# Performance work log

Measured on AMD Instinct MI355X. Metric: run time of the kernel, lower is better.

## Reference

```python
import jax, jax.numpy as jnp
import numpy as np

B, T, D, H, Dh, DF, MH = 4, 1024, 1024, 16, 64, 4096, 256
EPS = 1e-6


def setup_inputs() -> dict:
    key = jax.random.key(0)
    ks = jax.random.split(key, 10)
    s = 0.02
    w = lambda k, shape: jax.random.normal(k, shape, jnp.float32) * s
    return {
        "x": jax.random.normal(ks[0], (B, T, D), jnp.float32),
        "norm1_w": jnp.ones((D,), jnp.float32),
        "norm2_w": jnp.ones((D,), jnp.float32),
        "wq": w(ks[1], (D, D)),
        "wk": w(ks[2], (D, D)),
        "wv": w(ks[3], (D, D)),
        "wo": w(ks[4], (D, D)),
        "mnet_w1": w(ks[5], (D, MH)),
        "mnet_w2": w(ks[6], (MH, H * Dh)),
        "gate_w": w(ks[7], (D, DF)),
        "up_w": w(ks[8], (D, DF)),
        "down_w": w(ks[9], (DF, D)),
    }


def _rmsnorm(x, w):
    rms = jnp.sqrt(jnp.mean(x * x, axis=-1, keepdims=True) + EPS)
    return w * (x / rms)


def reference(x, norm1_w, norm2_w, wq, wk, wv, wo, mnet_w1, mnet_w2, gate_w, up_w, down_w):
    # --- pre-norm geodesic (DRM) attention ---
    h = _rmsnorm(x, norm1_w)  # [B,T,D]
    q = (h @ wq).reshape(B, T, H, Dh)
    k = (h @ wk).reshape(B, T, H, Dh)
    v = (h @ wv).reshape(B, T, H, Dh)
    # MetricNet: positive diagonal metric G(x) per token/head
    g = jax.nn.softplus(jax.nn.silu(h @ mnet_w1) @ mnet_w2).reshape(B, T, H, Dh)
    # squared geodesic distance under key-side diagonal metric, expanded form:
    # dist_ij = sum_d g_jd*(q_id - k_jd)^2 = q^2.g - 2 q.(g*k) + sum(g*k^2)
    gk = g * k
    dist = (
        jnp.einsum("bihd,bjhd->bhij", q * q, g)
        - 2.0 * jnp.einsum("bihd,bjhd->bhij", q, gk)
        + jnp.transpose(jnp.sum(gk * k, axis=-1), (0, 2, 1))[:, :, None, :]
    )  # [B,H,T,T]
    scores = -dist / np.float32(np.sqrt(Dh))
    causal = jnp.tril(jnp.ones((T, T), bool))
    scores = jnp.where(causal, scores, jnp.float32(-1e30))
    attn = jax.nn.softmax(scores, axis=-1)
    o = jnp.einsum("bhij,bjhd->bihd", attn, v).reshape(B, T, D) @ wo
    x = x + o
    # --- pre-norm SwiGLU FFN ---
    h2 = _rmsnorm(x, norm2_w)
    ffn = (jax.nn.silu(h2 @ gate_w) * (h2 @ up_w)) @ down_w
    return x + ffn
```

## Files before the change

kernel.cpp:

```cpp
#include <hip/hip_runtime.h>
#include <hip/hip_bf16.h>
#include <math.h>

#define BB  4
#define TT  1024
#define DD  1024
#define HH  16
#define DH  64
#define DFF 4096
#define MHH 256

typedef __attribute__((ext_vector_type(8))) short bf16x8;
typedef __attribute__((ext_vector_type(4))) float f32x4;
typedef unsigned int u32;

#define NEG_BIG (-1e9f)

__device__ __forceinline__ float b2f(short s) {
    union { unsigned int u; float f; } x;
    x.u = ((unsigned int)(unsigned short)s) << 16;
    return x.f;
}
__device__ __forceinline__ short f2b(float f) {
    union { float f; unsigned int u; } x; x.f = f;
    unsigned int r = x.u + 0x7fffu + ((x.u >> 16) & 1u);
    return (short)(r >> 16);
}
__device__ __forceinline__ float silu_f(float x) { return x / (1.f + __expf(-x)); }

__device__ __forceinline__ void gld16(const short* g, short* l) {
    __builtin_amdgcn_global_load_lds(
        (const __attribute__((address_space(1))) u32*)g,
        (__attribute__((address_space(3))) u32*)l, 16, 0, 0);
}

#define STAGE64(ga0, ga1, lds, kb)                                  \
    {                                                               \
        gld16((ga0) + (kb),      &(lds)[tid * 8]);                  \
        gld16((ga1) + (kb),      &(lds)[2048 + tid * 8]);           \
        gld16((ga0) + (kb) + 32, &(lds)[4096 + tid * 8]);           \
        gld16((ga1) + (kb) + 32, &(lds)[4096 + 2048 + tid * 8]);    \
    }

__device__ __forceinline__ void convT_tile_body(
    const float* __restrict__ src, short* __restrict__ dst,
    int K, int N, int bx, int by, int tid, short (*Ts)[36])
{
    const int k0 = by * 32, n0 = bx * 32;
    const int r = tid >> 3, c4 = (tid & 7) * 4;
    float4 v = *(const float4*)(src + (size_t)(k0 + r) * N + n0 + c4);
    Ts[r][c4 + 0] = f2b(v.x); Ts[r][c4 + 1] = f2b(v.y);
    Ts[r][c4 + 2] = f2b(v.z); Ts[r][c4 + 3] = f2b(v.w);
    __syncthreads();
    short4 o;
    o.x = Ts[c4 + 0][r]; o.y = Ts[c4 + 1][r];
    o.z = Ts[c4 + 2][r]; o.w = Ts[c4 + 3][r];
    *(short4*)(dst + (size_t)(n0 + r) * K + k0 + c4) = o;
}

__global__ __launch_bounds__(256) void convT_pre_k(
    const float* __restrict__ wq, const float* __restrict__ wk,
    const float* __restrict__ wv, const float* __restrict__ mw1,
    const float* __restrict__ wo, const float* __restrict__ mw2,
    short* __restrict__ WfT, short* __restrict__ woT, short* __restrict__ mw2T)
{
    __shared__ __align__(16) short Ts[32][36];
    const int b = blockIdx.x, tid = threadIdx.x;
    const float* src; short* dst; int K, N, bx, by;
    if (b < 1024)      { src = wq;  dst = WfT;               K = DD;  N = DD;  int l = b;        bx = l & 31; by = l >> 5; }
    else if (b < 2048) { src = wk;  dst = WfT + 1024 * 1024; K = DD;  N = DD;  int l = b - 1024; bx = l & 31; by = l >> 5; }
    else if (b < 3072) { src = wv;  dst = WfT + 2048 * 1024; K = DD;  N = DD;  int l = b - 2048; bx = l & 31; by = l >> 5; }
    else if (b < 3328) { src = mw1; dst = WfT + 3072 * 1024; K = DD;  N = MHH; int l = b - 3072; bx = l & 7;  by = l >> 3; }
    else if (b < 4352) { src = wo;  dst = woT;               K = DD;  N = DD;  int l = b - 3328; bx = l & 31; by = l >> 5; }
    else               { src = mw2; dst = mw2T;              K = MHH; N = DD;  int l = b - 4352; bx = l & 31; by = l >> 5; }
    convT_tile_body(src, dst, K, N, bx, by, tid, Ts);
}

__global__ __launch_bounds__(256) void convT_ffn_k(
    const float* __restrict__ gw, const float* __restrict__ uw,
    const float* __restrict__ dw,
    short* __restrict__ WgT, short* __restrict__ WuT, short* __restrict__ WdT)
{
    __shared__ __align__(16) short Ts[32][36];
    const int b = blockIdx.x, tid = threadIdx.x;
    const float* src; short* dst; int K, N, bx, by;
    if (b < 4096)      { src = gw; dst = WgT; K = DD;  N = DFF; int l = b;        bx = l & 127; by = l >> 7; }
    else if (b < 8192) { src = uw; dst = WuT; K = DD;  N = DFF; int l = b - 4096; bx = l & 127; by = l >> 7; }
    else               { src = dw; dst = WdT; K = DFF; N = DD;  int l = b - 8192; bx = l & 31;  by = l >> 5; }
    convT_tile_body(src, dst, K, N, bx, by, tid, Ts);
}

__global__ __launch_bounds__(256) void rmsnorm_k(
    const float* __restrict__ X, const float* __restrict__ W, short* __restrict__ O,
    float* __restrict__ XC)
{
    const int row = blockIdx.x;
    const int tid = threadIdx.x;
    float4 xv = ((const float4*)(X + (size_t)row * DD))[tid];
    if (XC) ((float4*)(XC + (size_t)row * DD))[tid] = xv;
    float f0 = xv.x, f1 = xv.y, f2 = xv.z, f3 = xv.w;
    float ss = f0*f0 + f1*f1 + f2*f2 + f3*f3;
    #pragma unroll
    for (int m = 1; m < 64; m <<= 1) ss += __shfl_xor(ss, m);
    __shared__ float red[4];
    if ((tid & 63) == 0) red[tid >> 6] = ss;
    __syncthreads();
    float tot = red[0] + red[1] + red[2] + red[3];
    float scale = rsqrtf(tot * (1.f / DD) + 1e-6f);
    float4 wv = ((const float4*)W)[tid];
    short4 ov;
    ov.x = f2b(f0 * scale * wv.x);
    ov.y = f2b(f1 * scale * wv.y);
    ov.z = f2b(f2 * scale * wv.z);
    ov.w = f2b(f3 * scale * wv.w);
    ((short4*)(O + (size_t)row * DD))[tid] = ov;
}

#define EP_NONE     0
#define EP_SILU     1
#define EP_SOFTPLUS 2
#define EP_RES      3

template<int EP, bool CF32, bool AUXF32>
__global__ __launch_bounds__(256, 4) void gemm128_k(
    const short* __restrict__ A, const short* __restrict__ Bt,
    void* Cv, const void* auxv,
    int N, int K, int lda, int ldb)
{
    __shared__ __align__(16) short As[2 * 4096];
    __shared__ __align__(16) short Bs[2 * 4096];
    const int tid  = threadIdx.x;
    const int wave = tid >> 6, lane = tid & 63;
    const int l16  = lane & 15, quad = lane >> 4;
    const int m0 = blockIdx.y * 128, n0 = blockIdx.x * 128;
    const int wm = (wave & 1) * 64, wn = (wave >> 1) * 64;

    f32x4 acc[4][4];
    #pragma unroll
    for (int i = 0; i < 4; i++)
        #pragma unroll
        for (int j = 0; j < 4; j++) acc[i][j] = (f32x4){0.f, 0.f, 0.f, 0.f};

    const int srow = tid >> 2, scol = (tid & 3) * 8;
    const short* ga0 = A  + (size_t)(m0 + srow)      * lda + scol;
    const short* ga1 = A  + (size_t)(m0 + 64 + srow) * lda + scol;
    const short* gb0 = Bt + (size_t)(n0 + srow)      * ldb + scol;
    const short* gb1 = Bt + (size_t)(n0 + 64 + srow) * ldb + scol;

    for (int kb = 0; kb < K; kb += 64) {
        STAGE64(ga0, ga1, As, kb);
        STAGE64(gb0, gb1, Bs, kb);
        __syncthreads();
        #pragma unroll
        for (int kc = 0; kc < 2; kc++) {
            bf16x8 af[4], bf[4];
            #pragma unroll
            for (int mi = 0; mi < 4; mi++)
                af[mi] = *(bf16x8*)&As[kc * 4096 + (wm + mi * 16 + l16) * 32 + quad * 8];
            #pragma unroll
            for (int ni = 0; ni < 4; ni++)
                bf[ni] = *(bf16x8*)&Bs[kc * 4096 + (wn + ni * 16 + l16) * 32 + quad * 8];
            #pragma unroll
            for (int mi = 0; mi < 4; mi++)
                #pragma unroll
                for (int ni = 0; ni < 4; ni++)
                    acc[mi][ni] = __builtin_amdgcn_mfma_f32_16x16x32_bf16(af[mi], bf[ni], acc[mi][ni], 0, 0, 0);
        }
        __syncthreads();
    }
    #pragma unroll
    for (int mi = 0; mi < 4; mi++) {
        #pragma unroll
        for (int ni = 0; ni < 4; ni++) {
            #pragma unroll
            for (int r = 0; r < 4; r++) {
                int row = m0 + wm + mi * 16 + quad * 4 + r;
                int col = n0 + wn + ni * 16 + l16;
                size_t idx = (size_t)row * N + col;
                float v = acc[mi][ni][r];
                if (EP == EP_SILU)          v = silu_f(v);
                else if (EP == EP_SOFTPLUS) v = fmaxf(v, 0.f) + log1pf(__expf(-fabsf(v)));
                else if (EP == EP_RES) {
                    if (AUXF32) v += ((const float*)auxv)[idx];
                    else        v += b2f(((const short*)auxv)[idx]);
                }
                if (CF32) ((float*)Cv)[idx] = v;
                else      ((short*)Cv)[idx] = f2b(v);
            }
        }
    }
}

__global__ __launch_bounds__(256, 4) void gemm128_atomic_k(
    const short* __restrict__ A, const short* __restrict__ Bt,
    float* out, int N, int Kc, int lda, int ldb)
{
    __shared__ __align__(16) short As[2 * 4096];
    __shared__ __align__(16) short Bs[2 * 4096];
    const int tid  = threadIdx.x;
    const int wave = tid >> 6, lane = tid & 63;
    const int l16  = lane & 15, quad = lane >> 4;
    const int m0 = blockIdx.y * 128, n0 = blockIdx.x * 128;
    const int wm = (wave & 1) * 64, wn = (wave >> 1) * 64;
    const int koff = blockIdx.z * Kc;

    f32x4 acc[4][4];
    #pragma unroll
    for (int i = 0; i < 4; i++)
        #pragma unroll
        for (int j = 0; j < 4; j++) acc[i][j] = (f32x4){0.f, 0.f, 0.f, 0.f};

    const int srow = tid >> 2, scol = (tid & 3) * 8;
    const short* ga0 = A  + (size_t)(m0 + srow)      * lda + koff + scol;
    const short* ga1 = A  + (size_t)(m0 + 64 + srow) * lda + koff + scol;
    const short* gb0 = Bt + (size_t)(n0 + srow)      * ldb + koff + scol;
    const short* gb1 = Bt + (size_t)(n0 + 64 + srow) * ldb + koff + scol;

    for (int kb = 0; kb < Kc; kb += 64) {
        STAGE64(ga0, ga1, As, kb);
        STAGE64(gb0, gb1, Bs, kb);
        __syncthreads();
        #pragma unroll
        for (int kc = 0; kc < 2; kc++) {
            bf16x8 af[4], bf[4];
            #pragma unroll
            for (int mi = 0; mi < 4; mi++)
                af[mi] = *(bf16x8*)&As[kc * 4096 + (wm + mi * 16 + l16) * 32 + quad * 8];
            #pragma unroll
            for (int ni = 0; ni < 4; ni++)
                bf[ni] = *(bf16x8*)&Bs[kc * 4096 + (wn + ni * 16 + l16) * 32 + quad * 8];
            #pragma unroll
            for (int mi = 0; mi < 4; mi++)
                #pragma unroll
                for (int ni = 0; ni < 4; ni++)
                    acc[mi][ni] = __builtin_amdgcn_mfma_f32_16x16x32_bf16(af[mi], bf[ni], acc[mi][ni], 0, 0, 0);
        }
        __syncthreads();
    }
    #pragma unroll
    for (int mi = 0; mi < 4; mi++)
        #pragma unroll
        for (int ni = 0; ni < 4; ni++)
            #pragma unroll
            for (int r = 0; r < 4; r++) {
                int row = m0 + wm + mi * 16 + quad * 4 + r;
                int col = n0 + wn + ni * 16 + l16;
                atomicAdd(out + (size_t)row * N + col, acc[mi][ni][r]);
            }
}

__global__ __launch_bounds__(256, 4) void gemm128_qkvm_k(
    const short* __restrict__ A, const short* __restrict__ Wf,
    short* __restrict__ Qb, short* __restrict__ Kb, short* __restrict__ Vb,
    short* __restrict__ M1)
{
    __shared__ __align__(16) short As[2 * 4096];
    __shared__ __align__(16) short Bs[2 * 4096];
    const int tid  = threadIdx.x;
    const int wave = tid >> 6, lane = tid & 63;
    const int l16  = lane & 15, quad = lane >> 4;
    const int m0 = blockIdx.y * 128, n0 = blockIdx.x * 128;
    const int wm = (wave & 1) * 64, wn = (wave >> 1) * 64;
    const int K = DD;

    f32x4 acc[4][4];
    #pragma unroll
    for (int i = 0; i < 4; i++)
        #pragma unroll
        for (int j = 0; j < 4; j++) acc[i][j] = (f32x4){0.f, 0.f, 0.f, 0.f};

    const int srow = tid >> 2, scol = (tid & 3) * 8;
    const short* ga0 = A  + (size_t)(m0 + srow)      * K + scol;
    const short* ga1 = A  + (size_t)(m0 + 64 + srow) * K + scol;
    const short* gb0 = Wf + (size_t)(n0 + srow)      * K + scol;
    const short* gb1 = Wf + (size_t)(n0 + 64 + srow) * K + scol;

    for (int kb = 0; kb < K; kb += 64) {
        STAGE64(ga0, ga1, As, kb);
        STAGE64(gb0, gb1, Bs, kb);
        __syncthreads();
        #pragma unroll
        for (int kc = 0; kc < 2; kc++) {
            bf16x8 af[4], bf[4];
            #pragma unroll
            for (int mi = 0; mi < 4; mi++)
                af[mi] = *(bf16x8*)&As[kc * 4096 + (wm + mi * 16 + l16) * 32 + quad * 8];
            #pragma unroll
            for (int ni = 0; ni < 4; ni++)
                bf[ni] = *(bf16x8*)&Bs[kc * 4096 + (wn + ni * 16 + l16) * 32 + quad * 8];
            #pragma unroll
            for (int mi = 0; mi < 4; mi++)
                #pragma unroll
                for (int ni = 0; ni < 4; ni++)
                    acc[mi][ni] = __builtin_amdgcn_mfma_f32_16x16x32_bf16(af[mi], bf[ni], acc[mi][ni], 0, 0, 0);
        }
        __syncthreads();
    }
    short* dst; int base, ldc; bool dosilu = false;
    if      (n0 < 1024) { dst = Qb; base = 0;    ldc = 1024; }
    else if (n0 < 2048) { dst = Kb; base = 1024; ldc = 1024; }
    else if (n0 < 3072) { dst = Vb; base = 2048; ldc = 1024; }
    else                { dst = M1; base = 3072; ldc = 256; dosilu = true; }
    #pragma unroll
    for (int mi = 0; mi < 4; mi++)
        #pragma unroll
        for (int ni = 0; ni < 4; ni++)
            #pragma unroll
            for (int r = 0; r < 4; r++) {
                int row = m0 + wm + mi * 16 + quad * 4 + r;
                int col = n0 + wn + ni * 16 + l16 - base;
                float v = acc[mi][ni][r];
                if (dosilu) v = silu_f(v);
                dst[(size_t)row * ldc + col] = f2b(v);
            }
}

__global__ __launch_bounds__(256, 2) void gemm128_swiglu_k(
    const short* __restrict__ A, const short* __restrict__ Gt,
    const short* __restrict__ Ut, short* __restrict__ F,
    int N, int K, int ldb)
{
    __shared__ __align__(16) short As[2 * 4096];
    __shared__ __align__(16) short Gs[2 * 4096];
    __shared__ __align__(16) short Us[2 * 4096];
    const int tid  = threadIdx.x;
    const int wave = tid >> 6, lane = tid & 63;
    const int l16  = lane & 15, quad = lane >> 4;

    int bx = blockIdx.x, by = blockIdx.y;
    {
        const int gx = gridDim.x;
        if ((gx & 7) == 0) {
            const int orig = by * gx + bx;
            const int xcd = orig & 7, j = orig >> 3;
            const int xpx = gx >> 3;
            bx = xcd * xpx + (j % xpx);
            by = j / xpx;
        }
    }
    const int m0 = by * 128, n0 = bx * 128;
    const int wm = (wave & 1) * 64, wn = (wave >> 1) * 64;

    f32x4 ag[4][4], au[4][4];
    #pragma unroll
    for (int i = 0; i < 4; i++)
        #pragma unroll
        for (int j = 0; j < 4; j++) {
            ag[i][j] = (f32x4){0.f, 0.f, 0.f, 0.f};
            au[i][j] = (f32x4){0.f, 0.f, 0.f, 0.f};
        }

    const int srow = tid >> 2, scol = (tid & 3) * 8;
    const short* ga0 = A  + (size_t)(m0 + srow)      * K   + scol;
    const short* ga1 = A  + (size_t)(m0 + 64 + srow) * K   + scol;
    const short* gg0 = Gt + (size_t)(n0 + srow)      * ldb + scol;
    const short* gg1 = Gt + (size_t)(n0 + 64 + srow) * ldb + scol;
    const short* gu0 = Ut + (size_t)(n0 + srow)      * ldb + scol;
    const short* gu1 = Ut + (size_t)(n0 + 64 + srow) * ldb + scol;

    for (int kb = 0; kb < K; kb += 64) {
        STAGE64(ga0, ga1, As, kb);
        STAGE64(gg0, gg1, Gs, kb);
        STAGE64(gu0, gu1, Us, kb);
        __syncthreads();
        #pragma unroll
        for (int kc = 0; kc < 2; kc++) {
            bf16x8 af[4], gf[4], uf[4];
            #pragma unroll
            for (int mi = 0; mi < 4; mi++)
                af[mi] = *(bf16x8*)&As[kc * 4096 + (wm + mi * 16 + l16) * 32 + quad * 8];
            #pragma unroll
            for (int ni = 0; ni < 4; ni++) {
                gf[ni] = *(bf16x8*)&Gs[kc * 4096 + (wn + ni * 16 + l16) * 32 + quad * 8];
                uf[ni] = *(bf16x8*)&Us[kc * 4096 + (wn + ni * 16 + l16) * 32 + quad * 8];
            }
            #pragma unroll
            for (int mi = 0; mi < 4; mi++)
                #pragma unroll
                for (int ni = 0; ni < 4; ni++) {
                    ag[mi][ni] = __builtin_amdgcn_mfma_f32_16x16x32_bf16(af[mi], gf[ni], ag[mi][ni], 0, 0, 0);
                    au[mi][ni] = __builtin_amdgcn_mfma_f32_16x16x32_bf16(af[mi], uf[ni], au[mi][ni], 0, 0, 0);
                }
        }
        __syncthreads();
    }
    #pragma unroll
    for (int mi = 0; mi < 4; mi++)
        #pragma unroll
        for (int ni = 0; ni < 4; ni++)
            #pragma unroll
            for (int r = 0; r < 4; r++) {
                int row = m0 + wm + mi * 16 + quad * 4 + r;
                int col = n0 + wn + ni * 16 + l16;
                F[(size_t)row * N + col] = f2b(silu_f(ag[mi][ni][r]) * au[mi][ni][r]);
            }
}

__global__ __launch_bounds__(256) void gkc_k(
    const short* __restrict__ G, short* KG,
    float* __restrict__ Cj)
{
    const int bt  = blockIdx.x;
    const int tid = threadIdx.x;
    const int h = tid >> 4, d0 = (tid & 15) * 4;
    const size_t base = (size_t)bt * (HH * DH) + h * DH + d0;
    short4 gv = *(const short4*)(G + base);
    short4 kv = *(const short4*)(KG + base);
    float g0 = b2f(gv.x), g1 = b2f(gv.y), g2 = b2f(gv.z), g3 = b2f(gv.w);
    float k0 = b2f(kv.x), k1 = b2f(kv.y), k2 = b2f(kv.z), k3 = b2f(kv.w);
    float p0 = g0*k0, p1 = g1*k1, p2 = g2*k2, p3 = g3*k3;
    short4 ov; ov.x = f2b(p0); ov.y = f2b(p1); ov.z = f2b(p2); ov.w = f2b(p3);
    *(short4*)(KG + base) = ov;
    float cc = p0*k0 + p1*k1 + p2*k2 + p3*k3;
    #pragma unroll
    for (int m = 1; m < 16; m <<= 1) cc += __shfl_xor(cc, m);
    if ((tid & 15) == 0) {
        int b = bt >> 10, t = bt & (TT - 1);
        Cj[((size_t)b * HH + h) * TT + t] = cc;
    }
}

__global__ __launch_bounds__(256) void attn_k(
    const short* __restrict__ Q, const short* __restrict__ G,
    const short* __restrict__ GK, const short* __restrict__ V,
    const float* __restrict__ Cj, short* __restrict__ O)
{
    __shared__ __align__(16) short Gs[64][72];
    __shared__ __align__(16) short GKs[64][72];
    __shared__ __align__(16) short Vt[64][72];
    __shared__ __align__(16) float Cs[64];
    __shared__ __align__(16) short Ps[4][16][72];

    const int pair = blockIdx.x;
    const int bh = blockIdx.y;
    const int b = bh >> 4, h = bh & 15;
    const int tid  = threadIdx.x;
    const int wave = tid >> 6, lane = tid & 63;
    const int l16  = lane & 15, quad = lane >> 4;

    const size_t bh_base = ((size_t)b * TT) * (HH * DH) + (size_t)h * DH;
    const float* cj_row = Cj + ((size_t)b * HH + h) * TT;

    const int sr2 = tid >> 3, sc2 = (tid & 7) * 8;
    const f32x4 z = {0.f, 0.f, 0.f, 0.f};

    for (int halfsel = 0; halfsel < 2; halfsel++) {
        const int it = halfsel ? 15 - pair : pair;
        const int i0 = it * 64;

        const int qrow = i0 + wave * 16 + l16;
        bf16x8 qf[2], qqf[2];
        #pragma unroll
        for (int kc = 0; kc < 2; kc++) {
            qf[kc] = *(const bf16x8*)(Q + bh_base + (size_t)qrow * (HH * DH) + kc * 32 + quad * 8);
            #pragma unroll
            for (int j = 0; j < 8; j++) {
                float f = b2f(qf[kc][j]);
                qqf[kc][j] = f2b(f * f);
            }
        }

        float m_i[4], l_i[4];
        f32x4 o_acc[4] = {z, z, z, z};
        #pragma unroll
        for (int r = 0; r < 4; r++) { m_i[r] = NEG_BIG; l_i[r] = 0.f; }

        for (int jt = 0; jt <= it; jt++) {
            const int j0 = jt * 64;
            #pragma unroll
            for (int pass = 0; pass < 2; pass++) {
                int jr = sr2 + pass * 32;
                size_t rb = bh_base + (size_t)(j0 + jr) * (HH * DH) + sc2;
                *(int4*)&Gs[jr][sc2]  = *(const int4*)(G + rb);
                *(int4*)&GKs[jr][sc2] = *(const int4*)(GK + rb);
                int4 vvec = *(const int4*)(V + rb);
                const short* vv = (const short*)&vvec;
                #pragma unroll
                for (int jj = 0; jj < 8; jj++) Vt[sc2 + jj][jr] = vv[jj];
            }
            if (tid < 64) Cs[tid] = cj_row[j0 + tid];
            __syncthreads();

            f32x4 s1[4] = {z, z, z, z}, s2[4] = {z, z, z, z};
            #pragma unroll
            for (int ns = 0; ns < 4; ns++) {
                #pragma unroll
                for (int kc = 0; kc < 2; kc++) {
                    bf16x8 gf  = *(bf16x8*)&Gs [ns * 16 + l16][kc * 32 + quad * 8];
                    bf16x8 gkf = *(bf16x8*)&GKs[ns * 16 + l16][kc * 32 + quad * 8];
                    s1[ns] = __builtin_amdgcn_mfma_f32_16x16x32_bf16(qqf[kc], gf,  s1[ns], 0, 0, 0);
                    s2[ns] = __builtin_amdgcn_mfma_f32_16x16x32_bf16(qf[kc],  gkf, s2[ns], 0, 0, 0);
                }
            }

            float p[4][4];
            #pragma unroll
            for (int ns = 0; ns < 4; ns++) {
                float cjv = Cs[ns * 16 + l16];
                #pragma unroll
                for (int r = 0; r < 4; r++)
                    p[ns][r] = (2.f * s2[ns][r] - s1[ns][r] - cjv) * 0.125f;
            }
            if (jt == it) {
                #pragma unroll
                for (int ns = 0; ns < 4; ns++) {
                    int j = j0 + ns * 16 + l16;
                    #pragma unroll
                    for (int r = 0; r < 4; r++) {
                        int i = i0 + wave * 16 + quad * 4 + r;
                        if (j > i) p[ns][r] = NEG_BIG;
                    }
                }
            }

            #pragma unroll
            for (int r = 0; r < 4; r++) {
                float mx = fmaxf(fmaxf(p[0][r], p[1][r]), fmaxf(p[2][r], p[3][r]));
                #pragma unroll
                for (int d2 = 1; d2 < 16; d2 <<= 1) mx = fmaxf(mx, __shfl_xor(mx, d2));
                float mnew = fmaxf(m_i[r], mx);
                float corr = __expf(m_i[r] - mnew);
                float sp = 0.f;
                #pragma unroll
                for (int ns = 0; ns < 4; ns++) {
                    float e = __expf(p[ns][r] - mnew);
                    p[ns][r] = e; sp += e;
                }
                #pragma unroll
                for (int d2 = 1; d2 < 16; d2 <<= 1) sp += __shfl_xor(sp, d2);
                l_i[r] = l_i[r] * corr + sp;
                m_i[r] = mnew;
                #pragma unroll
                for (int nv = 0; nv < 4; nv++) o_acc[nv][r] *= corr;
            }

            #pragma unroll
            for (int ns = 0; ns < 4; ns++)
                #pragma unroll
                for (int r = 0; r < 4; r++)
                    Ps[wave][quad * 4 + r][ns * 16 + l16] = f2b(p[ns][r]);

            bf16x8 pf[2];
            pf[0] = *(bf16x8*)&Ps[wave][l16][quad * 8];
            pf[1] = *(bf16x8*)&Ps[wave][l16][32 + quad * 8];
            #pragma unroll
            for (int nv = 0; nv < 4; nv++) {
                #pragma unroll
                for (int kc = 0; kc < 2; kc++) {
                    bf16x8 vf = *(bf16x8*)&Vt[nv * 16 + l16][kc * 32 + quad * 8];
                    o_acc[nv] = __builtin_amdgcn_mfma_f32_16x16x32_bf16(pf[kc], vf, o_acc[nv], 0, 0, 0);
                }
            }
            __syncthreads();
        }

        #pragma unroll
        for (int nv = 0; nv < 4; nv++) {
            #pragma unroll
            for (int r = 0; r < 4; r++) {
                int i = i0 + wave * 16 + quad * 4 + r;
                int d = nv * 16 + l16;
                O[bh_base + (size_t)i * (HH * DH) + d] = f2b(o_acc[nv][r] / l_i[r]);
            }
        }
    }
}

extern "C" void kernel_launch(void* const* d_in, const int* in_sizes, int n_in,
                              void* d_out, int out_size, void* d_ws, size_t ws_size,
                              hipStream_t stream)
{
    const float* x   = (const float*)d_in[0];
    const float* n1w = (const float*)d_in[1];
    const float* n2w = (const float*)d_in[2];
    const float* wq  = (const float*)d_in[3];
    const float* wk  = (const float*)d_in[4];
    const float* wv  = (const float*)d_in[5];
    const float* wo  = (const float*)d_in[6];
    const float* mw1 = (const float*)d_in[7];
    const float* mw2 = (const float*)d_in[8];
    const float* gw  = (const float*)d_in[9];
    const float* uw  = (const float*)d_in[10];
    const float* dw  = (const float*)d_in[11];
    float* out = (float*)d_out;

    const size_t MB = 1u << 20;
    if (ws_size < 48 * MB) return;
    const bool bigF = (ws_size >= 64 * MB);
    char* wsb = (char*)d_ws;
    short* h    = (short*)(wsb);
    short* g    = (short*)(wsb);
    short* h2   = (short*)(wsb);
    short* qb   = (short*)(wsb + 8 * MB);
    short* WgT  = (short*)(wsb + 8 * MB);
    short* kb   = (short*)(wsb + 16 * MB);
    short* WuT  = (short*)(wsb + 16 * MB);
    short* vb   = (short*)(wsb + 24 * MB);
    short* WdT  = (short*)(wsb + 24 * MB);
    short* WfT  = (short*)(wsb + 32 * MB);
    short* ob   = (short*)(wsb + 32 * MB);
    short* F    = (short*)(wsb + 32 * MB);
    short* woT  = (short*)(wsb + 40 * MB);
    short* m1   = (short*)(wsb + 42 * MB);
    float* cj   = (float*)(wsb + 44 * MB);
    short* mw2T = (short*)(wsb + 44 * MB + 512 * 1024);

    const int M = BB * TT;

    convT_pre_k<<<4608, 256, 0, stream>>>(wq, wk, wv, mw1, wo, mw2, WfT, woT, mw2T);

    rmsnorm_k<<<M, 256, 0, stream>>>(x, n1w, h, out);
    gemm128_qkvm_k<<<dim3(3328 / 128, M / 128), 256, 0, stream>>>(h, WfT, qb, kb, vb, m1);
    gemm128_k<EP_SOFTPLUS,false,false><<<dim3(DD / 128, M / 128), 256, 0, stream>>>(
        m1, mw2T, g, nullptr, DD, MHH, MHH, MHH);
    gkc_k<<<M, 256, 0, stream>>>(g, kb, cj);
    attn_k<<<dim3(8, BB * HH), 256, 0, stream>>>(qb, g, kb, vb, cj, ob);

    gemm128_atomic_k<<<dim3(DD / 128, M / 128, 2), 256, 0, stream>>>(
        ob, woT, out, DD, 512, DD, DD);

    rmsnorm_k<<<M, 256, 0, stream>>>(out, n2w, h2, nullptr);

    convT_ffn_k<<<12288, 256, 0, stream>>>(gw, uw, dw, WgT, WuT, WdT);

    if (bigF) {
        gemm128_swiglu_k<<<dim3(DFF / 128, M / 128), 256, 0, stream>>>(h2, WgT, WuT, F, DFF, DD, DD);
        gemm128_atomic_k<<<dim3(DD / 128, M / 128, 2), 256, 0, stream>>>(
            F, WdT, out, DD, 2048, DFF, DFF);
    } else {
        const int NH = DFF / 2;
        for (int half = 0; half < 2; half++) {
            gemm128_swiglu_k<<<dim3(NH / 128, M / 128), 256, 0, stream>>>(
                h2, WgT + (size_t)half * NH * DD, WuT + (size_t)half * NH * DD, F, NH, DD, DD);
            gemm128_atomic_k<<<dim3(DD / 128, M / 128, 2), 256, 0, stream>>>(
                F, WdT + (size_t)half * NH, out, DD, 1024, NH, DFF);
        }
    }
}
```

Measured before the change: 460.8 us.

## Use 256x256-tile 8-wave pipelined GEMMs for FFN swiglu and down projection

```diff
diff --git a/kernel.cpp b/kernel.cpp
--- a/kernel.cpp
+++ b/kernel.cpp
@@ -315,6 +315,175 @@
             }
 }
 
+#define G8_AF(BUF, MH)                                                         \
+    _Pragma("unroll")                                                          \
+    for (int mi2 = 0; mi2 < 4; mi2++) {                                        \
+        const int gr = rb + ((MH) * 4 + mi2) * 32 + l16;                       \
+        _Pragma("unroll")                                                      \
+        for (int kc = 0; kc < 2; kc++)                                         \
+            af[mi2][kc] = *(const bf16x8*)&LA[BUF][((gr >> 7) + kc * 2) * 4096 \
+                                + (gr & 127) * 32 + quad * 8];                 \
+    }
+
+#define G8_BF(BUF, NH)                                                         \
+    _Pragma("unroll")                                                          \
+    for (int ni2 = 0; ni2 < 2; ni2++) {                                        \
+        const int gc = cb + ((NH) * 2 + ni2) * 64 + l16;                       \
+        _Pragma("unroll")                                                      \
+        for (int kc = 0; kc < 2; kc++)                                         \
+            bf[ni2][kc] = *(const bf16x8*)&LB[BUF][((gc >> 7) + kc * 2) * 4096 \
+                                + (gc & 127) * 32 + quad * 8];                 \
+    }
+
+#define G8_MFMA(MH, NH)                                                        \
+    asm volatile("" ::: "memory");                                             \
+    __builtin_amdgcn_s_barrier();                                              \
+    asm volatile("" ::: "memory");                                             \
+    __builtin_amdgcn_s_setprio(1);                                             \
+    _Pragma("unroll")                                                          \
+    for (int mi2 = 0; mi2 < 4; mi2++)                                          \
+        _Pragma("unroll")                                                      \
+        for (int ni2 = 0; ni2 < 2; ni2++)                                      \
+            _Pragma("unroll")                                                  \
+            for (int kc = 0; kc < 2; kc++)                                     \
+                acc[(MH) * 4 + mi2][(NH) * 2 + ni2] =                          \
+                    __builtin_amdgcn_mfma_f32_16x16x32_bf16(af[mi2][kc],       \
+                        bf[ni2][kc], acc[(MH) * 4 + mi2][(NH) * 2 + ni2],      \
+                        0, 0, 0);                                              \
+    __builtin_amdgcn_s_setprio(0);                                             \
+    asm volatile("" ::: "memory");                                             \
+    __builtin_amdgcn_s_barrier();                                              \
+    asm volatile("" ::: "memory");
+
+#define G8_STAGE(p, L, h, kt)                                                  \
+    {                                                                          \
+        const short* s_ = (p) + (size_t)(kt) * 64;                             \
+        gld16(s_,      &(L)[(h) * 4096 + tid * 8]);                            \
+        gld16(s_ + 32, &(L)[(2 + (h)) * 4096 + tid * 8]);                      \
+    }
+
+#define G8_WAIT4 asm volatile("s_waitcnt vmcnt(4)" ::: "memory");
+#define G8_WAIT0 asm volatile("s_waitcnt vmcnt(0)" ::: "memory");
+
+#define G8_PROLOGUE                                                            \
+    G8_STAGE(gA0, LA[0], 0, 0); G8_STAGE(gA1, LA[0], 1, 0);                    \
+    G8_STAGE(gB0, LB[0], 0, 0); G8_STAGE(gB1, LB[0], 1, 0);                    \
+    G8_STAGE(gA0, LA[1], 0, 1); G8_STAGE(gB0, LB[1], 0, 1);                    \
+    G8_WAIT4                                                                   \
+    asm volatile("" ::: "memory");                                             \
+    __builtin_amdgcn_s_barrier();                                              \
+    asm volatile("" ::: "memory");
+
+#define G8_ITER                                                                \
+    {                                                                          \
+        bf16x8 af[4][2], bf[2][2];                                             \
+        G8_AF(0, 0);                                                           \
+        G8_BF(0, 0); G8_STAGE(gA1, LA[1], 1, t1); G8_MFMA(0, 0);               \
+        G8_BF(0, 1); G8_STAGE(gB1, LB[1], 1, t1); G8_MFMA(0, 1);               \
+        G8_AF(0, 1);                                                           \
+        G8_BF(0, 0); if (p2) G8_STAGE(gA0, LA[0], 0, t2); G8_MFMA(1, 0);       \
+        G8_BF(0, 1); if (p2) G8_STAGE(gB0, LB[0], 0, t2);                      \
+        if (p2) { G8_WAIT4 } else { G8_WAIT0 }                                 \
+        G8_MFMA(1, 1);                                                         \
+        G8_AF(1, 0);                                                           \
+        G8_BF(1, 0); if (p2) G8_STAGE(gA1, LA[0], 1, t2); G8_MFMA(0, 0);       \
+        G8_BF(1, 1); if (p2) G8_STAGE(gB1, LB[0], 1, t2); G8_MFMA(0, 1);       \
+        G8_AF(1, 1);                                                           \
+        G8_BF(1, 0); if (p2) G8_STAGE(gA0, LA[1], 0, t3); G8_MFMA(1, 0);       \
+        G8_BF(1, 1); if (p2) G8_STAGE(gB0, LB[1], 0, t3);                      \
+        if (p2) { G8_WAIT4 }                                                   \
+        G8_MFMA(1, 1);                                                         \
+    }
+
+__global__ __launch_bounds__(512, 2) void gemm256_atomic_k(
+    const short* __restrict__ A, const short* __restrict__ Bt,
+    float* out, int N, int Kc, int lda, int ldb)
+{
+    __shared__ __align__(16) short LA[2][16384];
+    __shared__ __align__(16) short LB[2][16384];
+    const int tid  = threadIdx.x;
+    const int wave = tid >> 6, lane = tid & 63;
+    const int l16  = lane & 15, quad = lane >> 4;
+    const int m0 = blockIdx.y * 256, n0 = blockIdx.x * 256;
+    const int rb = (wave >> 2) * 16, cb = (wave & 3) * 16;
+    const int koff = blockIdx.z * Kc;
+
+    f32x4 acc[8][4];
+    #pragma unroll
+    for (int i = 0; i < 8; i++)
+        #pragma unroll
+        for (int j = 0; j < 4; j++) acc[i][j] = (f32x4){0.f, 0.f, 0.f, 0.f};
+
+    const int srow = tid >> 2, scol = (tid & 3) * 8;
+    const short* gA0 = A  + (size_t)(m0 + srow)       * lda + koff + scol;
+    const short* gA1 = A  + (size_t)(m0 + 128 + srow) * lda + koff + scol;
+    const short* gB0 = Bt + (size_t)(n0 + srow)       * ldb + koff + scol;
+    const short* gB1 = Bt + (size_t)(n0 + 128 + srow) * ldb + koff + scol;
+
+    const int NT = Kc >> 6;
+    G8_PROLOGUE
+    for (int j = 0; j < (NT >> 1); j++) {
+        const int t1 = 2 * j + 1, t2 = t1 + 1, t3 = t1 + 2;
+        const bool p2 = t2 < NT;
+        G8_ITER
+    }
+    #pragma unroll
+    for (int mi = 0; mi < 8; mi++)
+        #pragma unroll
+        for (int ni = 0; ni < 4; ni++)
+            #pragma unroll
+            for (int r = 0; r < 4; r++) {
+                int row = m0 + rb + mi * 32 + quad * 4 + r;
+                int col = n0 + cb + ni * 64 + l16;
+                atomicAdd(out + (size_t)row * N + col, acc[mi][ni][r]);
+            }
+}
+
+__global__ __launch_bounds__(512, 2) void gemm256_swiglu_k(
+    const short* __restrict__ A, const short* __restrict__ Gt,
+    const short* __restrict__ Ut, short* __restrict__ F,
+    int N, int K, int ldb)
+{
+    __shared__ __align__(16) short LA[2][16384];
+    __shared__ __align__(16) short LB[2][16384];
+    const int tid  = threadIdx.x;
+    const int wave = tid >> 6, lane = tid & 63;
+    const int l16  = lane & 15, quad = lane >> 4;
+    const int m0 = blockIdx.y * 256, n0f = blockIdx.x * 128;
+    const int rb = (wave >> 2) * 16, cb = (wave & 3) * 16;
+
+    f32x4 acc[8][4];
+    #pragma unroll
+    for (int i = 0; i < 8; i++)
+        #pragma unroll
+        for (int j = 0; j < 4; j++) acc[i][j] = (f32x4){0.f, 0.f, 0.f, 0.f};
+
+    const int srow = tid >> 2, scol = (tid & 3) * 8;
+    const short* gA0 = A  + (size_t)(m0 + srow)       * K   + scol;
+    const short* gA1 = A  + (size_t)(m0 + 128 + srow) * K   + scol;
+    const short* gB0 = Gt + (size_t)(n0f + srow)      * ldb + scol;
+    const short* gB1 = Ut + (size_t)(n0f + srow)      * ldb + scol;
+
+    const int NT = K >> 6;
+    G8_PROLOGUE
+    for (int j = 0; j < (NT >> 1); j++) {
+        const int t1 = 2 * j + 1, t2 = t1 + 1, t3 = t1 + 2;
+        const bool p2 = t2 < NT;
+        G8_ITER
+    }
+    #pragma unroll
+    for (int mi = 0; mi < 8; mi++)
+        #pragma unroll
+        for (int ni2 = 0; ni2 < 2; ni2++)
+            #pragma unroll
+            for (int r = 0; r < 4; r++) {
+                int row = m0 + rb + mi * 32 + quad * 4 + r;
+                int col = n0f + cb + ni2 * 64 + l16;
+                F[(size_t)row * N + col] =
+                    f2b(silu_f(acc[mi][ni2][r]) * acc[mi][ni2 + 2][r]);
+            }
+}
+
 __global__ __launch_bounds__(256, 2) void gemm128_swiglu_k(
     const short* __restrict__ A, const short* __restrict__ Gt,
     const short* __restrict__ Ut, short* __restrict__ F,
@@ -327,18 +496,7 @@
     const int wave = tid >> 6, lane = tid & 63;
     const int l16  = lane & 15, quad = lane >> 4;
 
-    int bx = blockIdx.x, by = blockIdx.y;
-    {
-        const int gx = gridDim.x;
-        if ((gx & 7) == 0) {
-            const int orig = by * gx + bx;
-            const int xcd = orig & 7, j = orig >> 3;
-            const int xpx = gx >> 3;
-            bx = xcd * xpx + (j % xpx);
-            by = j / xpx;
-        }
-    }
-    const int m0 = by * 128, n0 = bx * 128;
+    const int m0 = blockIdx.y * 128, n0 = blockIdx.x * 128;
     const int wm = (wave & 1) * 64, wn = (wave >> 1) * 64;
 
     f32x4 ag[4][4], au[4][4];
@@ -624,9 +782,10 @@
     convT_ffn_k<<<12288, 256, 0, stream>>>(gw, uw, dw, WgT, WuT, WdT);
 
     if (bigF) {
-        gemm128_swiglu_k<<<dim3(DFF / 128, M / 128), 256, 0, stream>>>(h2, WgT, WuT, F, DFF, DD, DD);
-        gemm128_atomic_k<<<dim3(DD / 128, M / 128, 2), 256, 0, stream>>>(
-            F, WdT, out, DD, 2048, DFF, DFF);
+        gemm256_swiglu_k<<<dim3(DFF / 128, M / 256), 512, 0, stream>>>(
+            h2, WgT, WuT, F, DFF, DD, DD);
+        gemm256_atomic_k<<<dim3(DD / 256, M / 256, 4), 512, 0, stream>>>(
+            F, WdT, out, DD, 1024, DFF, DFF);
     } else {
         const int NH = DFF / 2;
         for (int half = 0; half < 2; half++) {
```

Result: slower. 506.7 us (+10.0%).
